# Performance work log

Hardware: AMD Instinct MI355X
Metric: run time of the kernel (lower is better)

The kernel has to match this reference:

```python
import jax, jax.numpy as jnp
import numpy as np

N_NODES = 100000
N_EDGES = 1600000
N_REL = 2
IN_CH, HID_CH, OUT_CH = 128, 128, 64


def setup_inputs() -> dict:
    key = jax.random.key(0)
    ks = jax.random.split(key, 8)
    x = jax.random.normal(ks[0], (N_NODES, IN_CH), dtype=jnp.float32)
    edge_index = jax.random.randint(ks[1], (2, N_EDGES), 0, N_NODES, dtype=jnp.int64)
    edge_type = jax.random.randint(ks[2], (N_EDGES,), 0, N_REL, dtype=jnp.int64)
    s1 = 1.0 / np.sqrt(IN_CH)
    s2 = 1.0 / np.sqrt(HID_CH)
    W1_rel = jax.random.normal(ks[3], (N_REL, IN_CH, HID_CH), dtype=jnp.float32) * s1
    W1_root = jax.random.normal(ks[4], (IN_CH, HID_CH), dtype=jnp.float32) * s1
    b1 = jnp.zeros((HID_CH,), dtype=jnp.float32)
    W2_rel = jax.random.normal(ks[5], (N_REL, HID_CH, OUT_CH), dtype=jnp.float32) * s2
    W2_root = jax.random.normal(ks[6], (HID_CH, OUT_CH), dtype=jnp.float32) * s2
    b2 = jnp.zeros((OUT_CH,), dtype=jnp.float32)
    return {"x": x, "edge_index": edge_index, "edge_type": edge_type,
            "W1_rel": W1_rel, "W1_root": W1_root, "b1": b1,
            "W2_rel": W2_rel, "W2_root": W2_root, "b2": b2}


def rgcn_conv(x, edge_index, edge_type, W_rel, W_root, b):
    """Relational graph conv: root transform + per-relation gather/matmul/scatter-mean."""
    src, dst = edge_index[0], edge_index[1]
    N = x.shape[0]
    out = x @ W_root + b  # self/root term
    x_src = x[src]  # [E, in] gather once, reused across relations
    for r in range(W_rel.shape[0]):  # N_REL is small and fixed
        mask = (edge_type == r)
        msg = jnp.where(mask[:, None], x_src, 0.0) @ W_rel[r]  # [E, out]
        agg = jax.ops.segment_sum(msg, dst, num_segments=N)  # [N, out]
        cnt = jax.ops.segment_sum(mask.astype(x.dtype), dst, num_segments=N)
        out = out + agg / jnp.maximum(cnt, 1.0)[:, None]  # mean aggregation
    return out


def l2_normalize(x, eps=1e-12):
    nrm = jnp.sqrt(jnp.sum(x * x, axis=1, keepdims=True))
    return x / jnp.maximum(nrm, eps)


def reference(x, edge_index, edge_type, W1_rel, W1_root, b1, W2_rel, W2_root, b2):
    h = jax.nn.relu(rgcn_conv(x, edge_index, edge_type, W1_rel, W1_root, b1))
    out = rgcn_conv(h, edge_index, edge_type, W2_rel, W2_root, b2)
    return l2_normalize(out)
```

## Files before the change

### kernel.cpp

```cpp
#include <hip/hip_runtime.h>
#include <hip/hip_bf16.h>


typedef unsigned int uint;
typedef unsigned short ushort;
typedef __attribute__((ext_vector_type(8))) short short8;
typedef __attribute__((ext_vector_type(16))) float floatx16;
typedef __attribute__((ext_vector_type(2))) float f32x2;

#define IN_CH  128
#define OUT_CH 64
#define SCAN_CHUNK 2048
#define EPB 8192
#define KPB 512
#define MAXBK 400

__device__ __forceinline__ ushort f2bf(float f) {
    uint u = __float_as_uint(f);
    u += 0x7FFF + ((u >> 16) & 1);
    return (ushort)(u >> 16);
}
__device__ __forceinline__ float bflo(uint u) { return __uint_as_float(u << 16); }
__device__ __forceinline__ float bfhi(uint u) { return __uint_as_float(u & 0xFFFF0000u); }


__global__ void k_count(const int* __restrict__ dst, const int* __restrict__ et,
                        int* __restrict__ cntblk, int E, int NBK, int NBLK) {
    __shared__ int cnt[MAXBK];
    int tid = threadIdx.x, blk = blockIdx.x;
    for (int b = tid; b < NBK; b += 256) cnt[b] = 0;
    __syncthreads();
    int base = blk * EPB;
#pragma unroll 4
    for (int i = 0; i < EPB / 256; i++) {
        int e = base + i * 256 + tid;
        if (e < E) {
            int key = 2 * dst[e] + et[e];
            atomicAdd(&cnt[key >> 9], 1);
        }
    }
    __syncthreads();
    for (int b = tid; b < NBK; b += 256) cntblk[b * NBLK + blk] = cnt[b];
}

__global__ void k_scan_a(const int* __restrict__ deg, int* __restrict__ offs,
                         int* __restrict__ bsums, int n) {
    __shared__ int sdata[256];
    int b = blockIdx.x, t = threadIdx.x;
    int base = b * SCAN_CHUNK + t * 8;
    int v[8];
    int sum = 0;
#pragma unroll
    for (int i = 0; i < 8; i++) {
        int idx = base + i;
        int x = (idx < n) ? deg[idx] : 0;
        v[i] = sum;
        sum += x;
    }
    sdata[t] = sum;
    __syncthreads();
    for (int ofs = 1; ofs < 256; ofs <<= 1) {
        int val = sdata[t];
        int add = (t >= ofs) ? sdata[t - ofs] : 0;
        __syncthreads();
        sdata[t] = val + add;
        __syncthreads();
    }
    int texcl = (t == 0) ? 0 : sdata[t - 1];
    if (t == 255) bsums[b] = sdata[255];
#pragma unroll
    for (int i = 0; i < 8; i++) {
        int idx = base + i;
        if (idx < n) offs[idx] = texcl + v[i];
    }
}

__global__ void k_scan_b(int* __restrict__ bsums, int* __restrict__ offs, int nb, int n) {
    int t = threadIdx.x;
    if (nb <= 64) {
        int v = (t < nb) ? bsums[t] : 0;
        int s = v;
#pragma unroll
        for (int d = 1; d < 64; d <<= 1) {
            int u = __shfl_up(s, d, 64);
            if (t >= d) s += u;
        }
        if (t < nb) bsums[t] = s - v;
        if (t == 63) offs[n] = s;
    } else if (t == 0) {
        int run = 0;
        for (int b = 0; b < nb; b++) {
            int x = bsums[b];
            bsums[b] = run;
            run += x;
        }
        offs[n] = run;
    }
}

__global__ void k_scan_c(int* __restrict__ offs, const int* __restrict__ bsums, int n) {
    int i = blockIdx.x * blockDim.x + threadIdx.x;
    if (i < n) offs[i] += bsums[i / SCAN_CHUNK];
}

__global__ void k_part(const int* __restrict__ src, const int* __restrict__ dst,
                       const int* __restrict__ et, const int* __restrict__ basebb,
                       uint* __restrict__ stage, int E, int NBK, int NBLK) {
    __shared__ int cnt[MAXBK];
    __shared__ int basel[MAXBK];
    int tid = threadIdx.x, blk = blockIdx.x;
    for (int b = tid; b < NBK; b += 256) {
        cnt[b] = 0;
        basel[b] = basebb[b * NBLK + blk];
    }
    __syncthreads();
    int base = blk * EPB;
#pragma unroll 4
    for (int i = 0; i < EPB / 256; i++) {
        int e = base + i * 256 + tid;
        if (e < E) {
            int s = src[e];
            int key = 2 * dst[e] + et[e];
            int bk = key >> 9;
            int r = atomicAdd(&cnt[bk], 1);
            stage[basel[bk] + r] = ((uint)(key & 511) << 23) | (uint)s;
        }
    }
}

__global__ void k_fine(const uint* __restrict__ stage, const int* __restrict__ basebb,
                       int* __restrict__ offs, int* __restrict__ esrc,
                       int E, int NBK, int NBLK) {
    __shared__ int kcnt[KPB];
    __shared__ int kcur[KPB];
    __shared__ int ssum[256];
    int tid = threadIdx.x, b = blockIdx.x;
    int start = basebb[b * NBLK];
    int endB = (b == NBK - 1) ? E : basebb[(b + 1) * NBLK];
    int size = endB - start;

    kcnt[tid] = 0;
    kcnt[tid + 256] = 0;
    __syncthreads();
    for (int i = tid; i < size; i += 256)
        atomicAdd(&kcnt[stage[start + i] >> 23], 1);
    __syncthreads();
    int v0 = kcnt[2 * tid], v1 = kcnt[2 * tid + 1];
    ssum[tid] = v0 + v1;
    __syncthreads();
    for (int ofs = 1; ofs < 256; ofs <<= 1) {
        int val = ssum[tid];
        int add = (tid >= ofs) ? ssum[tid - ofs] : 0;
        __syncthreads();
        ssum[tid] = val + add;
        __syncthreads();
    }
    int texcl = (tid == 0) ? 0 : ssum[tid - 1];
    kcur[2 * tid] = texcl;
    kcur[2 * tid + 1] = texcl + v0;
    offs[(b << 9) + 2 * tid] = start + texcl + v0;
    offs[(b << 9) + 2 * tid + 1] = start + texcl + v0 + v1;
    __syncthreads();
    for (int i = tid; i < size; i += 256) {
        uint p = stage[start + i];
        int r = atomicAdd(&kcur[p >> 23], 1);
        esrc[start + r] = (int)(p & 0x7FFFFFu);
    }
}


__global__ void k_cvt(const float* __restrict__ x, uint4* __restrict__ xb, int n8) {
    int i = blockIdx.x * 256 + threadIdx.x;
    if (i >= n8) return;
    const float4 f0 = ((const float4*)x)[(size_t)i * 2];
    const float4 f1 = ((const float4*)x)[(size_t)i * 2 + 1];
    uint4 o;
    o.x = (uint)f2bf(f0.x) | ((uint)f2bf(f0.y) << 16);
    o.y = (uint)f2bf(f0.z) | ((uint)f2bf(f0.w) << 16);
    o.z = (uint)f2bf(f1.x) | ((uint)f2bf(f1.y) << 16);
    o.w = (uint)f2bf(f1.z) | ((uint)f2bf(f1.w) << 16);
    xb[i] = o;
}


__device__ __forceinline__ uint4 pack8(const ushort* o) {
    uint4 v;
    v.x = (uint)o[0] | ((uint)o[1] << 16);
    v.y = (uint)o[2] | ((uint)o[3] << 16);
    v.z = (uint)o[4] | ((uint)o[5] << 16);
    v.w = (uint)o[6] | ((uint)o[7] << 16);
    return v;
}

__global__ void k_prep(const float* __restrict__ W1root, const float* __restrict__ W1rel,
                       const float* __restrict__ W2root, const float* __restrict__ W2rel,
                       uint4* __restrict__ Bpk1, uint4* __restrict__ Bpk2) {
    int idx = blockIdx.x * 256 + threadIdx.x;
    if (idx >= 10240) return;
    ushort o[8];
    if (idx < 6144) {
        int id = idx;
        int ct = id >> 11;
        int c = id & 2047;
        int gn = c >> 9, s = (c >> 6) & 7, h = (c >> 5) & 1, n = c & 31;
        int k0 = s * 16 + h * 8;
        int col = gn * 32 + n;
        const float* W = (ct == 0) ? W1root : (W1rel + (size_t)(ct - 1) * 16384);
#pragma unroll
        for (int j = 0; j < 8; j++) o[j] = f2bf(W[(k0 + j) * 128 + col]);
        Bpk1[id] = pack8(o);
    } else {
        int id = idx - 6144;
        int ct = id >> 11;
        int c = id & 2047;
        int gn = c >> 9, s = (c >> 6) & 7, h = (c >> 5) & 1, n = c & 31;
        int k0 = s * 16 + h * 8;
        int colg = ct * 128 + gn * 32 + n;
#pragma unroll
        for (int j = 0; j < 8; j++) {
            float f = 0.f;
            if (colg < 64)       f = W2root[(k0 + j) * 64 + colg];
            else if (colg < 128) f = W2rel[(k0 + j) * 64 + (colg - 64)];
            else if (colg < 192) f = W2rel[8192 + (k0 + j) * 64 + (colg - 128)];
            o[j] = f2bf(f);
        }
        Bpk2[id] = pack8(o);
    }
}


__global__ __launch_bounds__(256)
void k_agg(const int* __restrict__ offs, const int* __restrict__ esrc,
           const uint4* __restrict__ xb4, uint4* __restrict__ S4, int N) {
    int wid = (int)((blockIdx.x * 256L + threadIdx.x) >> 4);
    int c = threadIdx.x & 15;
    if (wid >= N) return;

    int beg0 = (wid == 0) ? 0 : offs[2 * wid - 1];
    int end0 = offs[2 * wid], end1 = offs[2 * wid + 1];

#pragma unroll
    for (int r = 0; r < 2; r++) {
        int beg = r ? end0 : beg0;
        int end = r ? end1 : end0;
        f32x2 a0 = {0.f, 0.f}, a1 = {0.f, 0.f}, a2 = {0.f, 0.f}, a3 = {0.f, 0.f};
        for (int c0 = beg; c0 < end; c0 += 16) {
            int myid = (c0 + c < end) ? esrc[c0 + c] : N;
            int m = min(16, end - c0);
            for (int eb = 0; eb < m; eb += 4) {
                uint4 v[4];
#pragma unroll
                for (int j = 0; j < 4; j++) {
                    int id = __shfl(myid, eb + j, 16);
                    v[j] = xb4[(uint)id * 16u + (uint)c];
                }
#pragma unroll
                for (int j = 0; j < 4; j++) {
                    a0 += (f32x2){bflo(v[j].x), bfhi(v[j].x)};
                    a1 += (f32x2){bflo(v[j].y), bfhi(v[j].y)};
                    a2 += (f32x2){bflo(v[j].z), bfhi(v[j].z)};
                    a3 += (f32x2){bflo(v[j].w), bfhi(v[j].w)};
                }
            }
        }
        float inv = (end > beg) ? 1.0f / (float)(end - beg) : 0.f;
        uint4 o;
        o.x = (uint)f2bf(a0.x * inv) | ((uint)f2bf(a0.y * inv) << 16);
        o.y = (uint)f2bf(a1.x * inv) | ((uint)f2bf(a1.y * inv) << 16);
        o.z = (uint)f2bf(a2.x * inv) | ((uint)f2bf(a2.y * inv) << 16);
        o.w = (uint)f2bf(a3.x * inv) | ((uint)f2bf(a3.y * inv) << 16);
        S4[(size_t)wid * 32 + r * 16 + c] = o;
    }
}


__global__ __launch_bounds__(256)
void k_gemm1(const ushort* __restrict__ xb, const ushort* __restrict__ S1,
             const ushort* __restrict__ Bpk, const float* __restrict__ b1,
             ushort* __restrict__ h, int N) {
    __shared__ ushort SH[32768];
    ushort* Alds = SH;
    ushort* Blds = SH + 16384;

    const int tid = threadIdx.x;
    const int lane = tid & 63;
    const int w = tid >> 6;
    const int wm = w >> 1, wn = w & 1;
    const int rowBase = blockIdx.x * 128;

    floatx16 acc[2][2] = {};

#pragma unroll
    for (int seg = 0; seg < 3; seg++) {
        const ushort* Ap = (seg == 0) ? xb : S1;
        const int stride = (seg == 0) ? 128 : 256;
        const int aoff = (seg == 2) ? 128 : 0;
        const uint4* Bsrc = (const uint4*)Bpk + seg * 2048;
#pragma unroll
        for (int i = 0; i < 8; i++) {
            int c = tid + i * 256;
            int m = c & 31, hh = (c >> 5) & 1, s = (c >> 6) & 7, g = c >> 9;
            int row = rowBase + g * 32 + m;
            if (row >= N) row = N - 1;
            int kc = s * 2 + hh;
            ((uint4*)Alds)[c] = *(const uint4*)(Ap + (size_t)row * stride + aoff + kc * 8);
            ((uint4*)Blds)[c] = Bsrc[c];
        }
        __syncthreads();
#pragma unroll
        for (int s = 0; s < 8; s++) {
            short8 a0 = *(const short8*)&Alds[(((wm * 2 + 0) * 8 + s) * 64 + lane) * 8];
            short8 a1 = *(const short8*)&Alds[(((wm * 2 + 1) * 8 + s) * 64 + lane) * 8];
            short8 b0 = *(const short8*)&Blds[(((wn * 2 + 0) * 8 + s) * 64 + lane) * 8];
            short8 b1f = *(const short8*)&Blds[(((wn * 2 + 1) * 8 + s) * 64 + lane) * 8];
            acc[0][0] = __builtin_amdgcn_mfma_f32_32x32x16_bf16(a0, b0, acc[0][0], 0, 0, 0);
            acc[0][1] = __builtin_amdgcn_mfma_f32_32x32x16_bf16(a0, b1f, acc[0][1], 0, 0, 0);
            acc[1][0] = __builtin_amdgcn_mfma_f32_32x32x16_bf16(a1, b0, acc[1][0], 0, 0, 0);
            acc[1][1] = __builtin_amdgcn_mfma_f32_32x32x16_bf16(a1, b1f, acc[1][1], 0, 0, 0);
        }
        __syncthreads();
    }

    ushort* Clds = SH;
    const int qr = 4 * (lane >> 5);
    const int cl = lane & 31;
    float bb[2];
#pragma unroll
    for (int nt = 0; nt < 2; nt++) bb[nt] = b1[wn * 64 + nt * 32 + cl];
#pragma unroll
    for (int mt = 0; mt < 2; mt++)
#pragma unroll
        for (int nt = 0; nt < 2; nt++) {
#pragma unroll
            for (int reg = 0; reg < 16; reg++) {
                int rl = (reg & 3) + 8 * (reg >> 2) + qr;
                float v = fmaxf(acc[mt][nt][reg] + bb[nt], 0.f);
                Clds[(wm * 64 + mt * 32 + rl) * 136 + wn * 64 + nt * 32 + cl] = f2bf(v);
            }
        }
    __syncthreads();

    int r = tid >> 1, half = tid & 1;
    int grow = rowBase + r;
    if (grow < N) {
#pragma unroll
        for (int k = 0; k < 8; k++) {
            int c0 = half * 64 + k * 8;
            uint4 v = *(const uint4*)&Clds[r * 136 + c0];
            *(uint4*)(h + (size_t)grow * 128 + c0) = v;
        }
    }
}


__global__ __launch_bounds__(256)
void k_gemmT(const ushort* __restrict__ A, const ushort* __restrict__ Bpk,
             ushort* __restrict__ Out, int N, int Ld) {
    __shared__ ushort SH[32768];
    ushort* Alds = SH;
    ushort* Blds = SH + 16384;

    const int tid = threadIdx.x;
    const int lane = tid & 63;
    const int w = tid >> 6;
    const int wm = w >> 1, wn = w & 1;
    const int rowBase = blockIdx.x * 128;
    const int ct = blockIdx.y;
    const int colBase = ct * 128;

    const uint4* Bsrc = (const uint4*)Bpk + (size_t)ct * 2048;
#pragma unroll
    for (int i = 0; i < 8; i++) {
        int c = tid + i * 256;
        ((uint4*)Blds)[c] = Bsrc[c];
    }
#pragma unroll
    for (int i = 0; i < 8; i++) {
        int c = tid + i * 256;
        int m = c & 31, h = (c >> 5) & 1, s = (c >> 6) & 7, g = c >> 9;
        int row = rowBase + g * 32 + m;
        if (row >= N) row = N - 1;
        int kc = s * 2 + h;
        ((uint4*)Alds)[c] = *(const uint4*)(A + (size_t)row * 128 + kc * 8);
    }
    __syncthreads();

    floatx16 acc[2][2] = {};
#pragma unroll
    for (int s = 0; s < 8; s++) {
        short8 a0 = *(const short8*)&Alds[(((wm * 2 + 0) * 8 + s) * 64 + lane) * 8];
        short8 a1 = *(const short8*)&Alds[(((wm * 2 + 1) * 8 + s) * 64 + lane) * 8];
        short8 b0 = *(const short8*)&Blds[(((wn * 2 + 0) * 8 + s) * 64 + lane) * 8];
        short8 b1 = *(const short8*)&Blds[(((wn * 2 + 1) * 8 + s) * 64 + lane) * 8];
        acc[0][0] = __builtin_amdgcn_mfma_f32_32x32x16_bf16(a0, b0, acc[0][0], 0, 0, 0);
        acc[0][1] = __builtin_amdgcn_mfma_f32_32x32x16_bf16(a0, b1, acc[0][1], 0, 0, 0);
        acc[1][0] = __builtin_amdgcn_mfma_f32_32x32x16_bf16(a1, b0, acc[1][0], 0, 0, 0);
        acc[1][1] = __builtin_amdgcn_mfma_f32_32x32x16_bf16(a1, b1, acc[1][1], 0, 0, 0);
    }
    __syncthreads();

    ushort* Clds = SH;
    const int qr = 4 * (lane >> 5);
    const int cl = lane & 31;
#pragma unroll
    for (int mt = 0; mt < 2; mt++)
#pragma unroll
        for (int nt = 0; nt < 2; nt++) {
#pragma unroll
            for (int reg = 0; reg < 16; reg++) {
                int rl = (reg & 3) + 8 * (reg >> 2) + qr;
                Clds[(wm * 64 + mt * 32 + rl) * 136 + wn * 64 + nt * 32 + cl] =
                    f2bf(acc[mt][nt][reg]);
            }
        }
    __syncthreads();

    int r = tid >> 1, half = tid & 1;
    int grow = rowBase + r;
    if (grow < N) {
#pragma unroll
        for (int k = 0; k < 8; k++) {
            int c0 = half * 64 + k * 8;
            int col = colBase + c0;
            if (col < Ld) {
                uint4 v = *(const uint4*)&Clds[r * 136 + c0];
                *(uint4*)(Out + (size_t)grow * Ld + col) = v;
            }
        }
    }
}


__global__ __launch_bounds__(256)
void k_final(const ushort* __restrict__ T2, const float* __restrict__ b2,
             const int* __restrict__ offs, const int* __restrict__ esrc,
             float* __restrict__ out, int N) {
    int wid = (int)((blockIdx.x * 256L + threadIdx.x) >> 3);
    int c = threadIdx.x & 7;
    if (wid >= N) return;
    const uint4* Tb = (const uint4*)T2;

    int beg0 = (wid == 0) ? 0 : offs[2 * wid - 1];
    int end0 = offs[2 * wid], end1 = offs[2 * wid + 1];

    f32x2 t0 = {0.f, 0.f}, t1 = {0.f, 0.f}, t2v = {0.f, 0.f}, t3v = {0.f, 0.f};
#pragma unroll
    for (int r = 0; r < 2; r++) {
        int beg = r ? end0 : beg0;
        int end = r ? end1 : end0;
        if (end > beg) {
            f32x2 a0 = {0.f, 0.f}, a1 = {0.f, 0.f}, a2 = {0.f, 0.f}, a3 = {0.f, 0.f};
            uint bc = 8u + 8u * (uint)r + (uint)c;
            for (int c0 = beg; c0 < end; c0 += 8) {
                int myid = (c0 + c < end) ? esrc[c0 + c] : N;
                int m = min(8, end - c0);
                for (int eb = 0; eb < m; eb += 4) {
                    uint4 v[4];
#pragma unroll
                    for (int j = 0; j < 4; j++) {
                        int id = __shfl(myid, eb + j, 8);
                        v[j] = Tb[(uint)id * 24u + bc];
                    }
#pragma unroll
                    for (int j = 0; j < 4; j++) {
                        a0 += (f32x2){bflo(v[j].x), bfhi(v[j].x)};
                        a1 += (f32x2){bflo(v[j].y), bfhi(v[j].y)};
                        a2 += (f32x2){bflo(v[j].z), bfhi(v[j].z)};
                        a3 += (f32x2){bflo(v[j].w), bfhi(v[j].w)};
                    }
                }
            }
            float inv = 1.0f / (float)(end - beg);
            t0 += a0 * inv; t1 += a1 * inv; t2v += a2 * inv; t3v += a3 * inv;
        }
    }
    uint4 ru = Tb[(uint)wid * 24u + (uint)c];
    float4 bbA = *(const float4*)(b2 + 8 * c);
    float4 bbB = *(const float4*)(b2 + 8 * c + 4);
    float v0 = bflo(ru.x) + bbA.x + t0.x;
    float v1 = bfhi(ru.x) + bbA.y + t0.y;
    float v2 = bflo(ru.y) + bbA.z + t1.x;
    float v3 = bfhi(ru.y) + bbA.w + t1.y;
    float v4 = bflo(ru.z) + bbB.x + t2v.x;
    float v5 = bfhi(ru.z) + bbB.y + t2v.y;
    float v6 = bflo(ru.w) + bbB.z + t3v.x;
    float v7 = bfhi(ru.w) + bbB.w + t3v.y;
    float sq = v0 * v0 + v1 * v1 + v2 * v2 + v3 * v3
             + v4 * v4 + v5 * v5 + v6 * v6 + v7 * v7;
#pragma unroll
    for (int d = 1; d <= 4; d <<= 1) sq += __shfl_xor(sq, d, 8);
    float rn = 1.0f / fmaxf(sqrtf(sq), 1e-12f);
    float4 oA = {v0 * rn, v1 * rn, v2 * rn, v3 * rn};
    float4 oB = {v4 * rn, v5 * rn, v6 * rn, v7 * rn};
    *(float4*)(out + (size_t)wid * 64 + 8 * c) = oA;
    *(float4*)(out + (size_t)wid * 64 + 8 * c + 4) = oB;
}


extern "C" void kernel_launch(void* const* d_in, const int* in_sizes, int n_in,
                              void* d_out, int out_size, void* d_ws, size_t ws_size,
                              hipStream_t stream) {
    const float* x      = (const float*)d_in[0];
    const int*   ei     = (const int*)d_in[1];
    const int*   etype  = (const int*)d_in[2];
    const float* W1rel  = (const float*)d_in[3];
    const float* W1root = (const float*)d_in[4];
    const float* b1     = (const float*)d_in[5];
    const float* W2rel  = (const float*)d_in[6];
    const float* W2root = (const float*)d_in[7];
    const float* b2     = (const float*)d_in[8];
    float* out = (float*)d_out;

    const int N = in_sizes[0] / IN_CH;
    const int E = in_sizes[2];
    const int NKEY = 2 * N;
    const int NBK  = (NKEY + KPB - 1) / KPB;
    const int NBLK = (E + EPB - 1) / EPB;
    const int NSC  = NBK * NBLK;

    const int* src = ei;
    const int* dst = ei + E;

    char* base = (char*)d_ws;
    size_t off = 0;
    auto carve = [&](size_t bytes) -> void* {
        void* p = base + off;
        off = (off + bytes + 511) & ~(size_t)511;
        return p;
    };
    ushort* xb    = (ushort*)carve((size_t)(N + 1) * 128 * sizeof(ushort));
    ushort* hA    = (ushort*)carve((size_t)N * 128 * sizeof(ushort));
    ushort* S1    = (ushort*)carve((size_t)N * 256 * sizeof(ushort));
    ushort* t2    = (ushort*)carve((size_t)(N + 1) * 192 * sizeof(ushort));
    int*    esrc  = (int*)carve((size_t)E * sizeof(int));
    uint*   stage = (uint*)carve((size_t)E * sizeof(uint));
    int*    offs  = (int*)carve((size_t)NBK * KPB * sizeof(int));
    int*    cntblk= (int*)carve((size_t)NSC * sizeof(int));
    int*    basebb= (int*)carve((size_t)(NSC + 1) * sizeof(int));
    int     NB    = (NSC + SCAN_CHUNK - 1) / SCAN_CHUNK;
    int*    bsums = (int*)carve((size_t)NB * sizeof(int));
    uint4*  Bpk1  = (uint4*)carve(6144 * sizeof(uint4));
    uint4*  Bpk2  = (uint4*)carve(4096 * sizeof(uint4));
    (void)ws_size; (void)n_in; (void)out_size;

    hipMemsetAsync(xb + (size_t)N * 128, 0, 128 * sizeof(ushort), stream);
    hipMemsetAsync(t2 + (size_t)N * 192, 0, 192 * sizeof(ushort), stream);

    k_count<<<NBLK, 256, 0, stream>>>(dst, etype, cntblk, E, NBK, NBLK);
    k_scan_a<<<NB, 256, 0, stream>>>(cntblk, basebb, bsums, NSC);
    k_scan_b<<<1, 64, 0, stream>>>(bsums, basebb, NB, NSC);
    k_scan_c<<<(NSC + 255) / 256, 256, 0, stream>>>(basebb, bsums, NSC);
    k_part<<<NBLK, 256, 0, stream>>>(src, dst, etype, basebb, stage, E, NBK, NBLK);
    k_fine<<<NBK, 256, 0, stream>>>(stage, basebb, offs, esrc, E, NBK, NBLK);

    int n8 = N * 16;
    k_cvt<<<(n8 + 255) / 256, 256, 0, stream>>>(x, (uint4*)xb, n8);
    k_prep<<<40, 256, 0, stream>>>(W1root, W1rel, W2root, W2rel, Bpk1, Bpk2);

    int rowTiles = (N + 127) / 128;
    int aggBlocks = (N + 15) / 16;
    int finBlocks = (N + 31) / 32;

    k_agg<<<aggBlocks, 256, 0, stream>>>(offs, esrc, (const uint4*)xb, (uint4*)S1, N);
    k_gemm1<<<rowTiles, 256, 0, stream>>>(xb, S1, (const ushort*)Bpk1, b1, hA, N);

    k_gemmT<<<dim3(rowTiles, 2), 256, 0, stream>>>(hA, (const ushort*)Bpk2, t2, N, 192);
    k_final<<<finBlocks, 256, 0, stream>>>(t2, b2, offs, esrc, out, N);
}
```

Baseline: 351.5 us.

## Fuse cvt/prep/memsets, drop scan_c, widen agg warps, single-pass gemmT over 192 columns

Merges the x conversion, weight packing and the two zero-row memsets into one launch, and folds the scan block-offset addition into k_part and k_fine so k_scan_c is removed. k_agg now uses 32 lanes per node that split edges into two halves and combine them with a shuffle, and it writes through nontemporal stores. k_gemmT computes all 192 output columns in one block instead of a 2-wide grid, so each A tile is loaded once. Other esrc loads and output stores become nontemporal. This cuts launch overhead and redundant A loads, at the cost of more LDS and registers in gemmT.

```diff
diff --git a/kernel.cpp b/kernel.cpp
--- a/kernel.cpp
+++ b/kernel.cpp
@@ -7,6 +7,8 @@
 typedef __attribute__((ext_vector_type(8))) short short8;
 typedef __attribute__((ext_vector_type(16))) float floatx16;
 typedef __attribute__((ext_vector_type(2))) float f32x2;
+typedef __attribute__((ext_vector_type(4))) float f32x4;
+typedef __attribute__((ext_vector_type(4))) uint u32x4;
 
 #define IN_CH  128
 #define OUT_CH 64
@@ -98,20 +100,17 @@
     }
 }
 
-__global__ void k_scan_c(int* __restrict__ offs, const int* __restrict__ bsums, int n) {
-    int i = blockIdx.x * blockDim.x + threadIdx.x;
-    if (i < n) offs[i] += bsums[i / SCAN_CHUNK];
-}
-
 __global__ void k_part(const int* __restrict__ src, const int* __restrict__ dst,
                        const int* __restrict__ et, const int* __restrict__ basebb,
+                       const int* __restrict__ bsums,
                        uint* __restrict__ stage, int E, int NBK, int NBLK) {
     __shared__ int cnt[MAXBK];
     __shared__ int basel[MAXBK];
     int tid = threadIdx.x, blk = blockIdx.x;
     for (int b = tid; b < NBK; b += 256) {
         cnt[b] = 0;
-        basel[b] = basebb[b * NBLK + blk];
+        int i = b * NBLK + blk;
+        basel[b] = basebb[i] + bsums[i >> 11];
     }
     __syncthreads();
     int base = blk * EPB;
@@ -129,14 +128,20 @@
 }
 
 __global__ void k_fine(const uint* __restrict__ stage, const int* __restrict__ basebb,
+                       const int* __restrict__ bsums,
                        int* __restrict__ offs, int* __restrict__ esrc,
                        int E, int NBK, int NBLK) {
     __shared__ int kcnt[KPB];
     __shared__ int kcur[KPB];
     __shared__ int ssum[256];
     int tid = threadIdx.x, b = blockIdx.x;
-    int start = basebb[b * NBLK];
-    int endB = (b == NBK - 1) ? E : basebb[(b + 1) * NBLK];
+    int i0 = b * NBLK;
+    int start = basebb[i0] + bsums[i0 >> 11];
+    int endB = E;
+    if (b != NBK - 1) {
+        int i1 = (b + 1) * NBLK;
+        endB = basebb[i1] + bsums[i1 >> 11];
+    }
     int size = endB - start;
 
     kcnt[tid] = 0;
@@ -166,20 +171,6 @@
         int r = atomicAdd(&kcur[p >> 23], 1);
         esrc[start + r] = (int)(p & 0x7FFFFFu);
     }
-}
-
-
-__global__ void k_cvt(const float* __restrict__ x, uint4* __restrict__ xb, int n8) {
-    int i = blockIdx.x * 256 + threadIdx.x;
-    if (i >= n8) return;
-    const float4 f0 = ((const float4*)x)[(size_t)i * 2];
-    const float4 f1 = ((const float4*)x)[(size_t)i * 2 + 1];
-    uint4 o;
-    o.x = (uint)f2bf(f0.x) | ((uint)f2bf(f0.y) << 16);
-    o.y = (uint)f2bf(f0.z) | ((uint)f2bf(f0.w) << 16);
-    o.z = (uint)f2bf(f1.x) | ((uint)f2bf(f1.y) << 16);
-    o.w = (uint)f2bf(f1.z) | ((uint)f2bf(f1.w) << 16);
-    xb[i] = o;
 }
 
 
@@ -192,85 +183,109 @@
     return v;
 }
 
-__global__ void k_prep(const float* __restrict__ W1root, const float* __restrict__ W1rel,
-                       const float* __restrict__ W2root, const float* __restrict__ W2rel,
-                       uint4* __restrict__ Bpk1, uint4* __restrict__ Bpk2) {
-    int idx = blockIdx.x * 256 + threadIdx.x;
-    if (idx >= 10240) return;
-    ushort o[8];
-    if (idx < 6144) {
-        int id = idx;
-        int ct = id >> 11;
-        int c = id & 2047;
-        int gn = c >> 9, s = (c >> 6) & 7, h = (c >> 5) & 1, n = c & 31;
-        int k0 = s * 16 + h * 8;
-        int col = gn * 32 + n;
-        const float* W = (ct == 0) ? W1root : (W1rel + (size_t)(ct - 1) * 16384);
-#pragma unroll
-        for (int j = 0; j < 8; j++) o[j] = f2bf(W[(k0 + j) * 128 + col]);
-        Bpk1[id] = pack8(o);
+__global__ void k_cvtprep(const float* __restrict__ x, uint4* __restrict__ xb, int n8,
+                          const float* __restrict__ W1root, const float* __restrict__ W1rel,
+                          const float* __restrict__ W2root, const float* __restrict__ W2rel,
+                          uint4* __restrict__ Bpk1, uint4* __restrict__ Bpk2,
+                          uint* __restrict__ xzero, uint* __restrict__ t2zero) {
+    int bid = blockIdx.x, tid = threadIdx.x;
+    if (bid < 40) {
+        if (bid == 0) {
+            if (tid < 64) xzero[tid] = 0;
+            if (tid < 96) t2zero[tid] = 0;
+        }
+        int idx = bid * 256 + tid;
+        ushort o[8];
+        if (idx < 6144) {
+            int id = idx;
+            int ct = id >> 11;
+            int c = id & 2047;
+            int gn = c >> 9, s = (c >> 6) & 7, h = (c >> 5) & 1, n = c & 31;
+            int k0 = s * 16 + h * 8;
+            int col = gn * 32 + n;
+            const float* W = (ct == 0) ? W1root : (W1rel + (size_t)(ct - 1) * 16384);
+#pragma unroll
+            for (int j = 0; j < 8; j++) o[j] = f2bf(W[(k0 + j) * 128 + col]);
+            Bpk1[id] = pack8(o);
+        } else {
+            int id = idx - 6144;
+            int ct = id >> 11;
+            int c = id & 2047;
+            int gn = c >> 9, s = (c >> 6) & 7, h = (c >> 5) & 1, n = c & 31;
+            int k0 = s * 16 + h * 8;
+            int colg = ct * 128 + gn * 32 + n;
+#pragma unroll
+            for (int j = 0; j < 8; j++) {
+                float f = 0.f;
+                if (colg < 64)       f = W2root[(k0 + j) * 64 + colg];
+                else if (colg < 128) f = W2rel[(k0 + j) * 64 + (colg - 64)];
+                else if (colg < 192) f = W2rel[8192 + (k0 + j) * 64 + (colg - 128)];
+                o[j] = f2bf(f);
+            }
+            Bpk2[id] = pack8(o);
+        }
     } else {
-        int id = idx - 6144;
-        int ct = id >> 11;
-        int c = id & 2047;
-        int gn = c >> 9, s = (c >> 6) & 7, h = (c >> 5) & 1, n = c & 31;
-        int k0 = s * 16 + h * 8;
-        int colg = ct * 128 + gn * 32 + n;
-#pragma unroll
-        for (int j = 0; j < 8; j++) {
-            float f = 0.f;
-            if (colg < 64)       f = W2root[(k0 + j) * 64 + colg];
-            else if (colg < 128) f = W2rel[(k0 + j) * 64 + (colg - 64)];
-            else if (colg < 192) f = W2rel[8192 + (k0 + j) * 64 + (colg - 128)];
-            o[j] = f2bf(f);
-        }
-        Bpk2[id] = pack8(o);
+        int i = (bid - 40) * 256 + tid;
+        if (i >= n8) return;
+        const f32x4* xp = (const f32x4*)x;
+        f32x4 f0 = __builtin_nontemporal_load(&xp[(size_t)i * 2]);
+        f32x4 f1 = __builtin_nontemporal_load(&xp[(size_t)i * 2 + 1]);
+        uint4 o;
+        o.x = (uint)f2bf(f0.x) | ((uint)f2bf(f0.y) << 16);
+        o.y = (uint)f2bf(f0.z) | ((uint)f2bf(f0.w) << 16);
+        o.z = (uint)f2bf(f1.x) | ((uint)f2bf(f1.y) << 16);
+        o.w = (uint)f2bf(f1.z) | ((uint)f2bf(f1.w) << 16);
+        xb[i] = o;
     }
 }
 
 
 __global__ __launch_bounds__(256)
 void k_agg(const int* __restrict__ offs, const int* __restrict__ esrc,
-           const uint4* __restrict__ xb4, uint4* __restrict__ S4, int N) {
-    int wid = (int)((blockIdx.x * 256L + threadIdx.x) >> 4);
-    int c = threadIdx.x & 15;
+           const uint4* __restrict__ xb4, uint* __restrict__ S, int N) {
+    int wid = (int)((blockIdx.x * 256L + threadIdx.x) >> 5);
+    int l = threadIdx.x & 31;
     if (wid >= N) return;
+    int q = l >> 4, c = l & 15;
 
     int beg0 = (wid == 0) ? 0 : offs[2 * wid - 1];
     int end0 = offs[2 * wid], end1 = offs[2 * wid + 1];
 
+    u32x4 o = {0, 0, 0, 0};
 #pragma unroll
     for (int r = 0; r < 2; r++) {
         int beg = r ? end0 : beg0;
         int end = r ? end1 : end0;
         f32x2 a0 = {0.f, 0.f}, a1 = {0.f, 0.f}, a2 = {0.f, 0.f}, a3 = {0.f, 0.f};
-        for (int c0 = beg; c0 < end; c0 += 16) {
-            int myid = (c0 + c < end) ? esrc[c0 + c] : N;
-            int m = min(16, end - c0);
+        for (int c0 = beg; c0 < end; c0 += 32) {
+            int myid = (c0 + l < end) ? __builtin_nontemporal_load(&esrc[c0 + l]) : N;
+            int m = min(32, end - c0);
             for (int eb = 0; eb < m; eb += 4) {
-                uint4 v[4];
-#pragma unroll
-                for (int j = 0; j < 4; j++) {
-                    int id = __shfl(myid, eb + j, 16);
-                    v[j] = xb4[(uint)id * 16u + (uint)c];
-                }
-#pragma unroll
-                for (int j = 0; j < 4; j++) {
-                    a0 += (f32x2){bflo(v[j].x), bfhi(v[j].x)};
-                    a1 += (f32x2){bflo(v[j].y), bfhi(v[j].y)};
-                    a2 += (f32x2){bflo(v[j].z), bfhi(v[j].z)};
-                    a3 += (f32x2){bflo(v[j].w), bfhi(v[j].w)};
+#pragma unroll
+                for (int j = 0; j < 2; j++) {
+                    int id = __shfl(myid, eb + 2 * j + q, 32);
+                    uint4 v = xb4[(uint)id * 16u + (uint)c];
+                    a0 += (f32x2){bflo(v.x), bfhi(v.x)};
+                    a1 += (f32x2){bflo(v.y), bfhi(v.y)};
+                    a2 += (f32x2){bflo(v.z), bfhi(v.z)};
+                    a3 += (f32x2){bflo(v.w), bfhi(v.w)};
                 }
             }
         }
-        float inv = (end > beg) ? 1.0f / (float)(end - beg) : 0.f;
-        uint4 o;
-        o.x = (uint)f2bf(a0.x * inv) | ((uint)f2bf(a0.y * inv) << 16);
-        o.y = (uint)f2bf(a1.x * inv) | ((uint)f2bf(a1.y * inv) << 16);
-        o.z = (uint)f2bf(a2.x * inv) | ((uint)f2bf(a2.y * inv) << 16);
-        o.w = (uint)f2bf(a3.x * inv) | ((uint)f2bf(a3.y * inv) << 16);
-        S4[(size_t)wid * 32 + r * 16 + c] = o;
-    }
+        a0.x += __shfl_xor(a0.x, 16, 32); a0.y += __shfl_xor(a0.y, 16, 32);
+        a1.x += __shfl_xor(a1.x, 16, 32); a1.y += __shfl_xor(a1.y, 16, 32);
+        a2.x += __shfl_xor(a2.x, 16, 32); a2.y += __shfl_xor(a2.y, 16, 32);
+        a3.x += __shfl_xor(a3.x, 16, 32); a3.y += __shfl_xor(a3.y, 16, 32);
+        if (q == r) {
+            float inv = (end > beg) ? 1.0f / (float)(end - beg) : 0.f;
+            o.x = (uint)f2bf(a0.x * inv) | ((uint)f2bf(a0.y * inv) << 16);
+            o.y = (uint)f2bf(a1.x * inv) | ((uint)f2bf(a1.y * inv) << 16);
+            o.z = (uint)f2bf(a2.x * inv) | ((uint)f2bf(a2.y * inv) << 16);
+            o.w = (uint)f2bf(a3.x * inv) | ((uint)f2bf(a3.y * inv) << 16);
+        }
+    }
+    u32x4* Sp = (u32x4*)S;
+    __builtin_nontemporal_store(o, &Sp[(size_t)wid * 32 + q * 16 + c]);
 }
 
 
@@ -355,8 +370,8 @@
 
 __global__ __launch_bounds__(256)
 void k_gemmT(const ushort* __restrict__ A, const ushort* __restrict__ Bpk,
-             ushort* __restrict__ Out, int N, int Ld) {
-    __shared__ ushort SH[32768];
+             ushort* __restrict__ Out, int N) {
+    __shared__ ushort SH[40960];
     ushort* Alds = SH;
     ushort* Blds = SH + 16384;
 
@@ -365,37 +380,38 @@
     const int w = tid >> 6;
     const int wm = w >> 1, wn = w & 1;
     const int rowBase = blockIdx.x * 128;
-    const int ct = blockIdx.y;
-    const int colBase = ct * 128;
-
-    const uint4* Bsrc = (const uint4*)Bpk + (size_t)ct * 2048;
+
+    const uint4* Bsrc = (const uint4*)Bpk;
+#pragma unroll
+    for (int i = 0; i < 12; i++) {
+        int c = tid + i * 256;
+        ((uint4*)Blds)[c] = Bsrc[c];
+    }
 #pragma unroll
     for (int i = 0; i < 8; i++) {
         int c = tid + i * 256;
-        ((uint4*)Blds)[c] = Bsrc[c];
-    }
-#pragma unroll
-    for (int i = 0; i < 8; i++) {
-        int c = tid + i * 256;
-        int m = c & 31, h = (c >> 5) & 1, s = (c >> 6) & 7, g = c >> 9;
+        int m = c & 31, hh = (c >> 5) & 1, s = (c >> 6) & 7, g = c >> 9;
         int row = rowBase + g * 32 + m;
         if (row >= N) row = N - 1;
-        int kc = s * 2 + h;
+        int kc = s * 2 + hh;
         ((uint4*)Alds)[c] = *(const uint4*)(A + (size_t)row * 128 + kc * 8);
     }
     __syncthreads();
 
-    floatx16 acc[2][2] = {};
+    floatx16 acc[2][3] = {};
 #pragma unroll
     for (int s = 0; s < 8; s++) {
         short8 a0 = *(const short8*)&Alds[(((wm * 2 + 0) * 8 + s) * 64 + lane) * 8];
         short8 a1 = *(const short8*)&Alds[(((wm * 2 + 1) * 8 + s) * 64 + lane) * 8];
-        short8 b0 = *(const short8*)&Blds[(((wn * 2 + 0) * 8 + s) * 64 + lane) * 8];
-        short8 b1 = *(const short8*)&Blds[(((wn * 2 + 1) * 8 + s) * 64 + lane) * 8];
+        short8 b0 = *(const short8*)&Blds[((wn * 3 + 0) * 512 + s * 64 + lane) * 8];
+        short8 b1 = *(const short8*)&Blds[((wn * 3 + 1) * 512 + s * 64 + lane) * 8];
+        short8 b2 = *(const short8*)&Blds[((wn * 3 + 2) * 512 + s * 64 + lane) * 8];
         acc[0][0] = __builtin_amdgcn_mfma_f32_32x32x16_bf16(a0, b0, acc[0][0], 0, 0, 0);
         acc[0][1] = __builtin_amdgcn_mfma_f32_32x32x16_bf16(a0, b1, acc[0][1], 0, 0, 0);
+        acc[0][2] = __builtin_amdgcn_mfma_f32_32x32x16_bf16(a0, b2, acc[0][2], 0, 0, 0);
         acc[1][0] = __builtin_amdgcn_mfma_f32_32x32x16_bf16(a1, b0, acc[1][0], 0, 0, 0);
         acc[1][1] = __builtin_amdgcn_mfma_f32_32x32x16_bf16(a1, b1, acc[1][1], 0, 0, 0);
+        acc[1][2] = __builtin_amdgcn_mfma_f32_32x32x16_bf16(a1, b2, acc[1][2], 0, 0, 0);
     }
     __syncthreads();
 
@@ -405,11 +421,11 @@
 #pragma unroll
     for (int mt = 0; mt < 2; mt++)
 #pragma unroll
-        for (int nt = 0; nt < 2; nt++) {
+        for (int nt = 0; nt < 3; nt++) {
 #pragma unroll
             for (int reg = 0; reg < 16; reg++) {
                 int rl = (reg & 3) + 8 * (reg >> 2) + qr;
-                Clds[(wm * 64 + mt * 32 + rl) * 136 + wn * 64 + nt * 32 + cl] =
+                Clds[(wm * 64 + mt * 32 + rl) * 200 + wn * 96 + nt * 32 + cl] =
                     f2bf(acc[mt][nt][reg]);
             }
         }
@@ -419,13 +435,10 @@
     int grow = rowBase + r;
     if (grow < N) {
 #pragma unroll
-        for (int k = 0; k < 8; k++) {
-            int c0 = half * 64 + k * 8;
-            int col = colBase + c0;
-            if (col < Ld) {
-                uint4 v = *(const uint4*)&Clds[r * 136 + c0];
-                *(uint4*)(Out + (size_t)grow * Ld + col) = v;
-            }
+        for (int k = 0; k < 12; k++) {
+            int c0 = half * 96 + k * 8;
+            uint4 v = *(const uint4*)&Clds[r * 200 + c0];
+            *(uint4*)(Out + (size_t)grow * 192 + c0) = v;
         }
     }
 }
@@ -452,7 +465,7 @@
             f32x2 a0 = {0.f, 0.f}, a1 = {0.f, 0.f}, a2 = {0.f, 0.f}, a3 = {0.f, 0.f};
             uint bc = 8u + 8u * (uint)r + (uint)c;
             for (int c0 = beg; c0 < end; c0 += 8) {
-                int myid = (c0 + c < end) ? esrc[c0 + c] : N;
+                int myid = (c0 + c < end) ? __builtin_nontemporal_load(&esrc[c0 + c]) : N;
                 int m = min(8, end - c0);
                 for (int eb = 0; eb < m; eb += 4) {
                     uint4 v[4];
@@ -490,10 +503,11 @@
 #pragma unroll
     for (int d = 1; d <= 4; d <<= 1) sq += __shfl_xor(sq, d, 8);
     float rn = 1.0f / fmaxf(sqrtf(sq), 1e-12f);
-    float4 oA = {v0 * rn, v1 * rn, v2 * rn, v3 * rn};
-    float4 oB = {v4 * rn, v5 * rn, v6 * rn, v7 * rn};
-    *(float4*)(out + (size_t)wid * 64 + 8 * c) = oA;
-    *(float4*)(out + (size_t)wid * 64 + 8 * c + 4) = oB;
+    f32x4 oA = {v0 * rn, v1 * rn, v2 * rn, v3 * rn};
+    f32x4 oB = {v4 * rn, v5 * rn, v6 * rn, v7 * rn};
+    f32x4* op = (f32x4*)(out + (size_t)wid * 64 + 8 * c);
+    __builtin_nontemporal_store(oA, op);
+    __builtin_nontemporal_store(oB, op + 1);
 }
 
 
@@ -543,27 +557,28 @@
     uint4*  Bpk2  = (uint4*)carve(4096 * sizeof(uint4));
     (void)ws_size; (void)n_in; (void)out_size;
 
-    hipMemsetAsync(xb + (size_t)N * 128, 0, 128 * sizeof(ushort), stream);
-    hipMemsetAsync(t2 + (size_t)N * 192, 0, 192 * sizeof(ushort), stream);
+    int n8 = N * 16;
+    int cvtBlocks = 40 + (n8 + 255) / 256;
+
+    k_cvtprep<<<cvtBlocks, 256, 0, stream>>>(x, (uint4*)xb, n8,
+                                             W1root, W1rel, W2root, W2rel,
+                                             Bpk1, Bpk2,
+                                             (uint*)(xb + (size_t)N * 128),
+                                             (uint*)(t2 + (size_t)N * 192));
 
     k_count<<<NBLK, 256, 0, stream>>>(dst, etype, cntblk, E, NBK, NBLK);
     k_scan_a<<<NB, 256, 0, stream>>>(cntblk, basebb, bsums, NSC);
     k_scan_b<<<1, 64, 0, stream>>>(bsums, basebb, NB, NSC);
-    k_scan_c<<<(NSC + 255) / 256, 256, 0, stream>>>(basebb, bsums, NSC);
-    k_part<<<NBLK, 256, 0, stream>>>(src, dst, etype, basebb, stage, E, NBK, NBLK);
-    k_fine<<<NBK, 256, 0, stream>>>(stage, basebb, offs, esrc, E, NBK, NBLK);
-
-    int n8 = N * 16;
-    k_cvt<<<(n8 + 255) / 256, 256, 0, stream>>>(x, (uint4*)xb, n8);
-    k_prep<<<40, 256, 0, stream>>>(W1root, W1rel, W2root, W2rel, Bpk1, Bpk2);
+    k_part<<<NBLK, 256, 0, stream>>>(src, dst, etype, basebb, bsums, stage, E, NBK, NBLK);
+    k_fine<<<NBK, 256, 0, stream>>>(stage, basebb, bsums, offs, esrc, E, NBK, NBLK);
 
     int rowTiles = (N + 127) / 128;
-    int aggBlocks = (N + 15) / 16;
+    int aggBlocks = (N + 7) / 8;
     int finBlocks = (N + 31) / 32;
 
-    k_agg<<<aggBlocks, 256, 0, stream>>>(offs, esrc, (const uint4*)xb, (uint4*)S1, N);
+    k_agg<<<aggBlocks, 256, 0, stream>>>(offs, esrc, (const uint4*)xb, (uint*)S1, N);
     k_gemm1<<<rowTiles, 256, 0, stream>>>(xb, S1, (const ushort*)Bpk1, b1, hA, N);
 
-    k_gemmT<<<dim3(rowTiles, 2), 256, 0, stream>>>(hA, (const ushort*)Bpk2, t2, N, 192);
+    k_gemmT<<<rowTiles, 256, 0, stream>>>(hA, (const ushort*)Bpk2, t2, N);
     k_final<<<finBlocks, 256, 0, stream>>>(t2, b2, offs, esrc, out, N);
 }
```

Result: no change. 349.8 us (-0.5%).
